# Performance work log

Hardware: AMD Instinct MI355X
Metric: run time of the kernel (lower is better)

The kernel has to match this reference:

```python
import jax, jax.numpy as jnp
import numpy as np

B, S, HID = 1, 4096, 2048
H, KV, D = 16, 8, 128
N_REP = H // KV
SCALING = float(128 ** -0.5)   # query_pre_attn_scalar ** -0.5
SOFTCAP = 50.0
WINDOW = 1024
NEG = -1e9


def setup_inputs() -> dict:
    key = jax.random.key(0)
    ks = jax.random.split(key, 6)
    hidden_states = jax.random.normal(ks[0], (B, S, HID), dtype=jnp.float32)
    Wq = jax.random.normal(ks[1], (HID, H * D), dtype=jnp.float32) * 0.02
    Wk = jax.random.normal(ks[2], (HID, KV * D), dtype=jnp.float32) * 0.02
    Wv = jax.random.normal(ks[3], (HID, KV * D), dtype=jnp.float32) * 0.02
    Wo = jax.random.normal(ks[4], (H * D, HID), dtype=jnp.float32) * 0.02
    # RoPE tables [1, S, D]
    inv_freq = 1.0 / (10000.0 ** (jnp.arange(0, D, 2, dtype=jnp.float32) / D))
    freqs = jnp.outer(jnp.arange(S, dtype=jnp.float32), inv_freq)   # [S, D/2]
    emb = jnp.concatenate([freqs, freqs], axis=-1)                  # [S, D]
    cos = jnp.cos(emb)[None]
    sin = jnp.sin(emb)[None]
    # causal + sliding-window additive mask [1, 1, S, S]
    i = jnp.arange(S)[:, None]
    j = jnp.arange(S)[None, :]
    allowed = (j <= i) & ((i - j) < WINDOW)
    attention_mask = jnp.where(allowed, 0.0, NEG).astype(jnp.float32)[None, None]
    return {"hidden_states": hidden_states, "cos": cos, "sin": sin,
            "attention_mask": attention_mask, "Wq": Wq, "Wk": Wk, "Wv": Wv, "Wo": Wo}


def _rotate_half(x):
    x1, x2 = jnp.split(x, 2, axis=-1)
    return jnp.concatenate([-x2, x1], axis=-1)


def reference(hidden_states, cos, sin, attention_mask, Wq, Wk, Wv, Wo):
    b, s, _ = hidden_states.shape
    # projections -> [B, heads, S, D]
    q = (hidden_states @ Wq).reshape(b, s, H, D).transpose(0, 2, 1, 3)
    k = (hidden_states @ Wk).reshape(b, s, KV, D).transpose(0, 2, 1, 3)
    v = (hidden_states @ Wv).reshape(b, s, KV, D).transpose(0, 2, 1, 3)
    # RoPE (unsqueeze_dim=1)
    c = cos[:, None]  # [B, 1, S, D]
    sn = sin[:, None]
    q = q * c + _rotate_half(q) * sn
    k = k * c + _rotate_half(k) * sn
    # repeat_kv (GQA)
    k = jnp.repeat(k, N_REP, axis=1)
    v = jnp.repeat(v, N_REP, axis=1)
    # scores with softcap + mask
    scores = jnp.einsum('bhqd,bhkd->bhqk', q, k) * SCALING
    scores = jnp.tanh(scores / SOFTCAP) * SOFTCAP
    scores = scores + attention_mask
    attn = jax.nn.softmax(scores.astype(jnp.float32), axis=-1).astype(q.dtype)
    out = jnp.einsum('bhqk,bhkd->bhqd', attn, v)
    out = out.transpose(0, 2, 1, 3).reshape(b, s, H * D)
    return out @ Wo
```

## Files before the change

### kernel.cpp

```cpp
#include <hip/hip_runtime.h>

#define S 4096
#define HID 2048
#define NH 16
#define NKV 8
#define HD 128
#define WINDOW 1024
#define SCALING 0.08838834764831845f
#define SOFTCAP 50.0f

typedef __bf16 bf16x8 __attribute__((ext_vector_type(8)));
typedef __bf16 bf16x4 __attribute__((ext_vector_type(4)));
typedef float f32x4 __attribute__((ext_vector_type(4)));

__device__ inline void gll16(const void* g, void* l) {
  __builtin_amdgcn_global_load_lds((const __attribute__((address_space(1))) void*)g,
                                   (__attribute__((address_space(3))) void*)l, 16, 0, 0);
}

__global__ void prep_all(const float* __restrict__ hs, __bf16* __restrict__ hsb,
                         const float* __restrict__ Wq, const float* __restrict__ Wk,
                         const float* __restrict__ Wv, const float* __restrict__ Wo,
                         __bf16* __restrict__ wqkvT, __bf16* __restrict__ woT) {
  int b = blockIdx.x;
  int t = threadIdx.x;
  if (b < 8192) {
    int i = b * 256 + t;
    float4 v = ((const float4*)hs)[i];
    bf16x4 o;
    o[0] = (__bf16)v.x; o[1] = (__bf16)v.y; o[2] = (__bf16)v.z; o[3] = (__bf16)v.w;
    ((bf16x4*)hsb)[i] = o;
    return;
  }
  __shared__ float tile[64][65];
  int y = b - 8192;
  int k0 = (y & 31) * 64;
  int wy = y >> 5;
  const float* src; __bf16* dst; int Nsrc, c0, perm, n0;
  if (wy < 32)      { src = Wq; dst = wqkvT; Nsrc = 2048; c0 = wy * 64;        perm = 1; n0 = wy * 64; }
  else if (wy < 48) { src = Wk; dst = wqkvT; Nsrc = 1024; c0 = (wy - 32) * 64; perm = 1; n0 = 2048 + (wy - 32) * 64; }
  else if (wy < 64) { src = Wv; dst = wqkvT; Nsrc = 1024; c0 = (wy - 48) * 64; perm = 0; n0 = 3072 + (wy - 48) * 64; }
  else              { src = Wo; dst = woT;   Nsrc = 2048; c0 = (wy - 64) * 64; perm = 0; n0 = (wy - 64) * 64; }
#pragma unroll
  for (int e = 0; e < 16; ++e) {
    int f = e * 256 + t; int r = f >> 6, c = f & 63;
    tile[r][c] = src[(size_t)(k0 + r) * Nsrc + c0 + c];
  }
  __syncthreads();
#pragma unroll
  for (int e = 0; e < 16; ++e) {
    int f = e * 256 + t; int r = f >> 6, c = f & 63;
    int n = n0 + r;
    if (perm) {
      int d = n & 127, o = d >> 4;
      int g = (o < 4) ? (o * 2) : ((o - 4) * 2 + 1);
      n = (n & ~127) | (g << 4) | (d & 15);
    }
    dst[(size_t)n * 2048 + k0 + c] = (__bf16)tile[c][r];
  }
}

__global__ __launch_bounds__(256) void gemm_qkv(const __bf16* __restrict__ A,
                                                const __bf16* __restrict__ B,
                                                __bf16* __restrict__ qr,
                                                __bf16* __restrict__ kr,
                                                __bf16* __restrict__ vt,
                                                const float* __restrict__ cosp,
                                                const float* __restrict__ sinp) {
  __shared__ __align__(16) __bf16 As[128 * 64];
  __shared__ __align__(16) __bf16 Bs[128 * 64];
  const int K = 2048;
  int m0 = blockIdx.x * 128, n0 = blockIdx.y * 128;
  int t = threadIdx.x;
  int lane = t & 63, wave = t >> 6;
  int wm = wave & 1, wn = wave >> 1;
  int quad = lane >> 4, l16 = lane & 15;

  f32x4 acc[4][4] = {};

  const __bf16* Abase = A + (size_t)m0 * K;
  const __bf16* Bbase = B + (size_t)n0 * K;

  for (int kk = 0; kk < K; kk += 64) {
    __syncthreads();
#pragma unroll
    for (int i = 0; i < 4; ++i) {
      int idx = i * 256 + t;
      int row = idx >> 3, c = idx & 7;
      int g = (c ^ (row & 7)) * 8;
      gll16(Abase + (size_t)row * K + kk + g, &As[idx * 8]);
      gll16(Bbase + (size_t)row * K + kk + g, &Bs[idx * 8]);
    }
    __syncthreads();
#pragma unroll
    for (int ks = 0; ks < 64; ks += 32) {
      bf16x8 af[4], bfr[4];
#pragma unroll
      for (int i = 0; i < 4; ++i) {
        int row = wm * 64 + i * 16 + l16;
        af[i] = *(const bf16x8*)&As[row * 64 + (((quad + (ks >> 3)) ^ (row & 7)) * 8)];
      }
#pragma unroll
      for (int j = 0; j < 4; ++j) {
        int row = wn * 64 + j * 16 + l16;
        bfr[j] = *(const bf16x8*)&Bs[row * 64 + (((quad + (ks >> 3)) ^ (row & 7)) * 8)];
      }
#pragma unroll
      for (int i = 0; i < 4; ++i)
#pragma unroll
        for (int j = 0; j < 4; ++j)
          acc[i][j] = __builtin_amdgcn_mfma_f32_16x16x32_bf16(af[i], bfr[j], acc[i][j], 0, 0, 0);
    }
  }

  if (n0 < 3072) {
    __bf16* dst = (n0 < 2048) ? (qr + (size_t)(n0 >> 7) * S * 128)
                              : (kr + (size_t)((n0 - 2048) >> 7) * S * 128);
#pragma unroll
    for (int i = 0; i < 4; ++i)
#pragma unroll
      for (int r = 0; r < 4; ++r) {
        int row = m0 + wm * 64 + i * 16 + quad * 4 + r;
#pragma unroll
        for (int jp = 0; jp < 2; ++jp) {
          int ifr = (wn * 2 + jp) * 16 + l16;
          float c = cosp[(size_t)row * 128 + ifr];
          float sn = sinp[(size_t)row * 128 + ifr];
          float lo = acc[i][2 * jp][r], hi = acc[i][2 * jp + 1][r];
          dst[(size_t)row * 128 + wn * 64 + jp * 32 + l16]      = (__bf16)(lo * c - hi * sn);
          dst[(size_t)row * 128 + wn * 64 + jp * 32 + 16 + l16] = (__bf16)(hi * c + lo * sn);
        }
      }
  } else {
    int vc0 = n0 - 3072;
#pragma unroll
    for (int i = 0; i < 4; ++i)
#pragma unroll
      for (int j = 0; j < 4; ++j) {
        int row_base = m0 + wm * 64 + i * 16 + quad * 4;
        int col = vc0 + wn * 64 + j * 16 + l16;
        bf16x4 ov;
#pragma unroll
        for (int r = 0; r < 4; ++r) ov[r] = (__bf16)acc[i][j][r];
        *(bf16x4*)&vt[(size_t)col * S + row_base] = ov;
      }
  }
}

template <typename OutT>
__global__ __launch_bounds__(256) void gemm_bt(const __bf16* __restrict__ A,
                                               const __bf16* __restrict__ B,
                                               OutT* __restrict__ C, int N, int K) {
  __shared__ __align__(16) __bf16 As[128 * 64];
  __shared__ __align__(16) __bf16 Bs[128 * 64];
  int m0 = blockIdx.x * 128, n0 = blockIdx.y * 128;
  int t = threadIdx.x;
  int lane = t & 63, wave = t >> 6;
  int wm = wave & 1, wn = wave >> 1;
  int quad = lane >> 4, l16 = lane & 15;

  f32x4 acc[4][4] = {};

  const __bf16* Abase = A + (size_t)m0 * K;
  const __bf16* Bbase = B + (size_t)n0 * K;

  for (int kk = 0; kk < K; kk += 64) {
    __syncthreads();
#pragma unroll
    for (int i = 0; i < 4; ++i) {
      int idx = i * 256 + t;
      int row = idx >> 3, c = idx & 7;
      int g = (c ^ (row & 7)) * 8;
      gll16(Abase + (size_t)row * K + kk + g, &As[idx * 8]);
      gll16(Bbase + (size_t)row * K + kk + g, &Bs[idx * 8]);
    }
    __syncthreads();
#pragma unroll
    for (int ks = 0; ks < 64; ks += 32) {
      bf16x8 af[4], bfr[4];
#pragma unroll
      for (int i = 0; i < 4; ++i) {
        int row = wm * 64 + i * 16 + l16;
        af[i] = *(const bf16x8*)&As[row * 64 + (((quad + (ks >> 3)) ^ (row & 7)) * 8)];
      }
#pragma unroll
      for (int j = 0; j < 4; ++j) {
        int row = wn * 64 + j * 16 + l16;
        bfr[j] = *(const bf16x8*)&Bs[row * 64 + (((quad + (ks >> 3)) ^ (row & 7)) * 8)];
      }
#pragma unroll
      for (int i = 0; i < 4; ++i)
#pragma unroll
        for (int j = 0; j < 4; ++j)
          acc[i][j] = __builtin_amdgcn_mfma_f32_16x16x32_bf16(af[i], bfr[j], acc[i][j], 0, 0, 0);
    }
  }
#pragma unroll
  for (int i = 0; i < 4; ++i)
#pragma unroll
    for (int j = 0; j < 4; ++j)
#pragma unroll
      for (int r = 0; r < 4; ++r) {
        int row = m0 + wm * 64 + i * 16 + quad * 4 + r;
        int col = n0 + wn * 64 + j * 16 + l16;
        C[(size_t)row * N + col] = (OutT)acc[i][j][r];
      }
}

__global__ __launch_bounds__(512) void attn(const __bf16* __restrict__ qr,
                                            const __bf16* __restrict__ kr,
                                            const __bf16* __restrict__ vt,
                                            __bf16* __restrict__ ao) {
  __shared__ __align__(16) __bf16 Ks[2][64 * 128];
  __shared__ __align__(16) __bf16 Vs[3][128 * 64];

  int kvh = blockIdx.x;
  int q0 = blockIdx.y * 128;
  int t = threadIdx.x, lane = t & 63, wave = t >> 6;
  int quad = lane >> 4, l16 = lane & 15;
  int h = kvh * 2 + (wave & 1);
  int qbase = q0 + (wave >> 1) * 32;

  bf16x8 qf[2][4];
#pragma unroll
  for (int mi = 0; mi < 2; ++mi) {
    const __bf16* qptr = qr + ((size_t)h * S + qbase + mi * 16 + l16) * 128;
#pragma unroll
    for (int ks = 0; ks < 4; ++ks)
      qf[mi][ks] = *(const bf16x8*)&qptr[ks * 32 + quad * 8];
  }

  f32x4 o[2][8] = {};
  float lpart[2] = {0.f, 0.f};

  int lo = q0 - (WINDOW - 1); if (lo < 0) lo = 0;
  int kt_begin = (lo / 64) * 64;
  int kt_end = q0 + 128;
  int NT = (kt_end - kt_begin) >> 6;

  const __bf16* kbase0 = kr + (size_t)kvh * S * 128;
  const __bf16* vbase0 = vt + (size_t)kvh * 128 * S;

  float4 k0r[2], k1r[2];
  float2 v0a[2], v0b[2], v1a[2], v1b[2];

  auto load_regs = [&](int kt, float4 (&krg)[2], float2 (&va)[2], float2 (&vb)[2]) {
    const __bf16* kb = kbase0 + (size_t)kt * 128;
    const __bf16* vptr = vbase0 + kt;
#pragma unroll
    for (int i = 0; i < 2; ++i) {
      int off = i * 512 + t;
      krg[i] = *(const float4*)(kb + (size_t)off * 8);
      int r = off >> 3, c = off & 7;
      int base0 = 32 * (c >> 2) + 4 * (c & 3);
      va[i] = *(const float2*)(vptr + (size_t)r * S + base0);
      vb[i] = *(const float2*)(vptr + (size_t)r * S + base0 + 16);
    }
  };
  auto write_lds = [&](int kslot, int vslot, float4 (&krg)[2], float2 (&va)[2], float2 (&vb)[2]) {
#pragma unroll
    for (int i = 0; i < 2; ++i) {
      int off = i * 512 + t;
      { int r = off >> 4, c = off & 15;
        *(float4*)&Ks[kslot][r * 128 + ((c ^ (r & 15)) * 8)] = krg[i]; }
      { int r = off >> 3, c = off & 7;
        float4 v = {va[i].x, va[i].y, vb[i].x, vb[i].y};
        *(float4*)&Vs[vslot][r * 64 + ((c ^ (r & 7)) * 8)] = v; }
    }
  };

  const float XS = SCALING / SOFTCAP;
  f32x4 sA[2][4], sB[2][4];

  auto activ = [&](int kt0) {
    return !(kt0 > qbase + 31 || kt0 + 63 < qbase - (WINDOW - 1));
  };

  auto step = [&](int tt, f32x4 (&SC)[2][4], f32x4 (&SP)[2][4], int vr, int vw,
                  float4 (&krl)[2], float2 (&val)[2], float2 (&vbl)[2],
                  float4 (&krs)[2], float2 (&vas)[2], float2 (&vbs)[2]) {
    if (tt < NT) {
      int kt0 = kt_begin + tt * 64;
      if (activ(kt0)) {
        int kslot = tt & 1;
#pragma unroll
        for (int mi = 0; mi < 2; ++mi)
#pragma unroll
          for (int nt = 0; nt < 4; ++nt) SC[mi][nt] = {};
        __builtin_amdgcn_s_setprio(1);
#pragma unroll
        for (int nt = 0; nt < 4; ++nt) {
#pragma unroll
          for (int ks = 0; ks < 4; ++ks) {
            bf16x8 kf = *(const bf16x8*)&Ks[kslot][(nt * 16 + l16) * 128 + (((ks * 4 + quad) ^ l16) * 8)];
            SC[0][nt] = __builtin_amdgcn_mfma_f32_16x16x32_bf16(kf, qf[0][ks], SC[0][nt], 0, 0, 0);
            SC[1][nt] = __builtin_amdgcn_mfma_f32_16x16x32_bf16(kf, qf[1][ks], SC[1][nt], 0, 0, 0);
          }
        }
        __builtin_amdgcn_s_setprio(0);
      }
    }

    if (tt + 2 < NT) load_regs(kt_begin + (tt + 2) * 64, krl, val, vbl);

    if (tt > 0) {
      int kt0c = kt_begin + (tt - 1) * 64;
      if (activ(kt0c)) {
        bf16x4 pk[2][4];
        bool interior = (kt0c + 63 <= qbase) && (kt0c >= qbase + 31 - (WINDOW - 1));
#pragma unroll
        for (int mi = 0; mi < 2; ++mi) {
          int irow = qbase + mi * 16 + l16;
#pragma unroll
          for (int nt = 0; nt < 4; ++nt)
#pragma unroll
            for (int r = 0; r < 4; ++r) {
              float x = SP[mi][nt][r] * XS;
              x = fminf(fmaxf(x, -0.25f), 0.25f);
              float x2 = x * x;
              float th = x * fmaf(x2, fmaf(x2, 0.13333333f, -0.33333333f), 1.0f);
              float pp = __builtin_amdgcn_exp2f(fmaf(th, 72.134752f, -72.134752f));
              if (!interior) {
                int j = kt0c + nt * 16 + quad * 4 + r;
                bool ok = (j <= irow) && (irow - j < WINDOW);
                pp = ok ? pp : 0.0f;
              }
              lpart[mi] += pp;
              pk[mi][nt][r] = (__bf16)pp;
            }
        }

        bf16x8 pB[2][2];
#pragma unroll
        for (int mi = 0; mi < 2; ++mi)
#pragma unroll
          for (int ks = 0; ks < 2; ++ks)
#pragma unroll
            for (int e = 0; e < 4; ++e) {
              pB[mi][ks][e]     = pk[mi][2 * ks][e];
              pB[mi][ks][4 + e] = pk[mi][2 * ks + 1][e];
            }

        __builtin_amdgcn_s_setprio(1);
#pragma unroll
        for (int dt = 0; dt < 8; ++dt) {
          int row = dt * 16 + l16;
#pragma unroll
          for (int ks = 0; ks < 2; ++ks) {
            bf16x8 vf = *(const bf16x8*)&Vs[vr][row * 64 + (((ks * 4 + quad) ^ (l16 & 7)) * 8)];
#pragma unroll
            for (int mi = 0; mi < 2; ++mi)
              o[mi][dt] = __builtin_amdgcn_mfma_f32_16x16x32_bf16(vf, pB[mi][ks], o[mi][dt], 0, 0, 0);
          }
        }
        __builtin_amdgcn_s_setprio(0);
      }
    }

    if (tt + 1 < NT) write_lds((tt + 1) & 1, vw, krs, vas, vbs);
    __syncthreads();
  };

  load_regs(kt_begin, k0r, v0a, v0b);
  write_lds(0, 0, k0r, v0a, v0b);
  if (NT > 1) load_regs(kt_begin + 64, k1r, v1a, v1b);
  __syncthreads();

  int vw = 1, vr = 2;
  for (int tt = 0; tt < NT; tt += 2) {
    step(tt, sA, sB, vr, vw, k0r, v0a, v0b, k1r, v1a, v1b);
    if (++vw == 3) vw = 0; if (++vr == 3) vr = 0;
    step(tt + 1, sB, sA, vr, vw, k1r, v1a, v1b, k0r, v0a, v0b);
    if (++vw == 3) vw = 0; if (++vr == 3) vr = 0;
  }
  step(NT, sA, sB, vr, vw, k0r, v0a, v0b, k1r, v1a, v1b);

#pragma unroll
  for (int mi = 0; mi < 2; ++mi) {
    float ls = lpart[mi];
    ls += __shfl_xor(ls, 16);
    ls += __shfl_xor(ls, 32);
    float inv = 1.f / ls;
    int row = qbase + mi * 16 + l16;
    __bf16* dst = ao + (size_t)row * (NH * HD) + h * HD + quad * 4;
#pragma unroll
    for (int dt = 0; dt < 8; ++dt) {
      bf16x4 ov;
#pragma unroll
      for (int r = 0; r < 4; ++r) ov[r] = (__bf16)(o[mi][dt][r] * inv);
      *(bf16x4*)(dst + dt * 16) = ov;
    }
  }
}

extern "C" void kernel_launch(void* const* d_in, const int* in_sizes, int n_in,
                              void* d_out, int out_size, void* d_ws, size_t ws_size,
                              hipStream_t stream) {
  const float* hs   = (const float*)d_in[0];
  const float* cosp = (const float*)d_in[1];
  const float* sinp = (const float*)d_in[2];
  const float* Wq = (const float*)d_in[4];
  const float* Wk = (const float*)d_in[5];
  const float* Wv = (const float*)d_in[6];
  const float* Wo = (const float*)d_in[7];
  float* out = (float*)d_out;

  char* w = (char*)d_ws;
  __bf16* hsb   = (__bf16*)w; w += (size_t)S * HID * 2;
  __bf16* wqkvT = (__bf16*)w; w += (size_t)4096 * 2048 * 2;
  __bf16* woT   = (__bf16*)w; w += (size_t)2048 * 2048 * 2;
  __bf16* qr    = (__bf16*)w; w += (size_t)NH * S * HD * 2;
  __bf16* kr    = (__bf16*)w; w += (size_t)NKV * S * HD * 2;
  __bf16* vtb   = (__bf16*)w; w += (size_t)NKV * HD * S * 2;
  __bf16* ao    = hsb;

  prep_all<<<8192 + 3072, 256, 0, stream>>>(hs, hsb, Wq, Wk, Wv, Wo, wqkvT, woT);

  gemm_qkv<<<dim3(32, 32), 256, 0, stream>>>(hsb, wqkvT, qr, kr, vtb, cosp, sinp);

  attn<<<dim3(NKV, 32), 512, 0, stream>>>(qr, kr, vtb, ao);

  gemm_bt<float><<<dim3(32, 16), 256, 0, stream>>>(ao, woT, out, 2048, 2048);
}
```

Before: 359.7 us.

## Enlarge QKV GEMM tile to 256x256 with double-buffered LDS pipeline

The QKV projection GEMM moves from 128x128 tiles with 4 waves to 256x256 tiles with 8 waves. LDS is double-buffered, and the loads for the next K tile are interleaved with MFMA phases, using s_setprio and barriers. The goal is to hide global-load latency and raise arithmetic intensity per block. In exchange, LDS use grows to 128KB and register pressure rises, and with only 256 blocks the launch may not fill all CUs evenly.

```diff
diff --git a/kernel.cpp b/kernel.cpp
--- a/kernel.cpp
+++ b/kernel.cpp
@@ -60,88 +60,129 @@
   }
 }
 
-__global__ __launch_bounds__(256) void gemm_qkv(const __bf16* __restrict__ A,
+__global__ __launch_bounds__(512) void gemm_qkv(const __bf16* __restrict__ A,
                                                 const __bf16* __restrict__ B,
                                                 __bf16* __restrict__ qr,
                                                 __bf16* __restrict__ kr,
                                                 __bf16* __restrict__ vt,
                                                 const float* __restrict__ cosp,
                                                 const float* __restrict__ sinp) {
-  __shared__ __align__(16) __bf16 As[128 * 64];
-  __shared__ __align__(16) __bf16 Bs[128 * 64];
+  __shared__ __align__(16) __bf16 As[2][2][128 * 64];
+  __shared__ __align__(16) __bf16 Bs[2][2][128 * 64];
   const int K = 2048;
-  int m0 = blockIdx.x * 128, n0 = blockIdx.y * 128;
+  const int NT = K / 64;
+  int m0 = blockIdx.x * 256, n0 = blockIdx.y * 256;
   int t = threadIdx.x;
   int lane = t & 63, wave = t >> 6;
   int wm = wave & 1, wn = wave >> 1;
   int quad = lane >> 4, l16 = lane & 15;
 
-  f32x4 acc[4][4] = {};
+  f32x4 acc[8][4] = {};
 
   const __bf16* Abase = A + (size_t)m0 * K;
   const __bf16* Bbase = B + (size_t)n0 * K;
 
-  for (int kk = 0; kk < K; kk += 64) {
-    __syncthreads();
-#pragma unroll
-    for (int i = 0; i < 4; ++i) {
-      int idx = i * 256 + t;
+  auto stageA = [&](int buf, int half, int kt) {
+    const __bf16* src = Abase + (size_t)(half * 128) * K + kt * 64;
+#pragma unroll
+    for (int j = 0; j < 2; ++j) {
+      int idx = j * 512 + t;
       int row = idx >> 3, c = idx & 7;
       int g = (c ^ (row & 7)) * 8;
-      gll16(Abase + (size_t)row * K + kk + g, &As[idx * 8]);
-      gll16(Bbase + (size_t)row * K + kk + g, &Bs[idx * 8]);
-    }
-    __syncthreads();
-#pragma unroll
-    for (int ks = 0; ks < 64; ks += 32) {
-      bf16x8 af[4], bfr[4];
-#pragma unroll
-      for (int i = 0; i < 4; ++i) {
-        int row = wm * 64 + i * 16 + l16;
-        af[i] = *(const bf16x8*)&As[row * 64 + (((quad + (ks >> 3)) ^ (row & 7)) * 8)];
-      }
-#pragma unroll
-      for (int j = 0; j < 4; ++j) {
-        int row = wn * 64 + j * 16 + l16;
-        bfr[j] = *(const bf16x8*)&Bs[row * 64 + (((quad + (ks >> 3)) ^ (row & 7)) * 8)];
-      }
-#pragma unroll
-      for (int i = 0; i < 4; ++i)
-#pragma unroll
-        for (int j = 0; j < 4; ++j)
-          acc[i][j] = __builtin_amdgcn_mfma_f32_16x16x32_bf16(af[i], bfr[j], acc[i][j], 0, 0, 0);
-    }
+      gll16(src + (size_t)row * K + g, &As[buf][half][idx * 8]);
+    }
+  };
+  auto stageB = [&](int buf, int half, int kt) {
+    const __bf16* src = Bbase + (size_t)(half * 128) * K + kt * 64;
+#pragma unroll
+    for (int j = 0; j < 2; ++j) {
+      int idx = j * 512 + t;
+      int row = idx >> 3, c = idx & 7;
+      int g = (c ^ (row & 7)) * 8;
+      gll16(src + (size_t)row * K + g, &Bs[buf][half][idx * 8]);
+    }
+  };
+
+  bf16x8 af[8];
+
+  auto readA = [&](int buf, int mi, int ks) -> bf16x8 {
+    int row = mi * 16 + l16;
+    return *(const bf16x8*)&As[buf][wm][row * 64 + (((quad + ks * 4) ^ (row & 7)) * 8)];
+  };
+  auto readB = [&](int buf, int ni, int ks) -> bf16x8 {
+    int row = (wn & 1) * 64 + ni * 16 + l16;
+    return *(const bf16x8*)&Bs[buf][wn >> 1][row * 64 + (((quad + ks * 4) ^ (row & 7)) * 8)];
+  };
+
+  auto phase = [&](int buf, int q, auto&& stage_fn) {
+    int ks = q >> 1, nip = q & 1;
+    if (nip == 0) {
+#pragma unroll
+      for (int mi = 0; mi < 8; ++mi) af[mi] = readA(buf, mi, ks);
+    }
+    bf16x8 b0 = readB(buf, 2 * nip, ks);
+    bf16x8 b1 = readB(buf, 2 * nip + 1, ks);
+    stage_fn();
+    __builtin_amdgcn_s_barrier();
+    __builtin_amdgcn_s_setprio(1);
+#pragma unroll
+    for (int mi = 0; mi < 8; ++mi) {
+      acc[mi][2 * nip]     = __builtin_amdgcn_mfma_f32_16x16x32_bf16(af[mi], b0, acc[mi][2 * nip], 0, 0, 0);
+      acc[mi][2 * nip + 1] = __builtin_amdgcn_mfma_f32_16x16x32_bf16(af[mi], b1, acc[mi][2 * nip + 1], 0, 0, 0);
+    }
+    __builtin_amdgcn_s_setprio(0);
+    __builtin_amdgcn_s_barrier();
+  };
+
+  stageA(0, 0, 0); stageA(0, 1, 0); stageB(0, 0, 0); stageB(0, 1, 0);
+  asm volatile("s_waitcnt vmcnt(0)" ::: "memory");
+  __builtin_amdgcn_s_barrier();
+  __builtin_amdgcn_sched_barrier(0);
+
+  for (int kt = 0; kt < NT; ++kt) {
+    int buf = kt & 1, nbuf = buf ^ 1;
+    bool st = (kt + 1 < NT);
+    int ktn = kt + 1;
+    phase(buf, 0, [&] { if (st) stageA(nbuf, 0, ktn); });
+    phase(buf, 1, [&] { if (st) stageA(nbuf, 1, ktn); });
+    phase(buf, 2, [&] { if (st) stageB(nbuf, 0, ktn); });
+    phase(buf, 3, [&] { if (st) stageB(nbuf, 1, ktn); });
+    asm volatile("s_waitcnt vmcnt(0)" ::: "memory");
+    __builtin_amdgcn_s_barrier();
+    __builtin_amdgcn_sched_barrier(0);
   }
 
   if (n0 < 3072) {
-    __bf16* dst = (n0 < 2048) ? (qr + (size_t)(n0 >> 7) * S * 128)
-                              : (kr + (size_t)((n0 - 2048) >> 7) * S * 128);
-#pragma unroll
-    for (int i = 0; i < 4; ++i)
+    int nf = n0 + wn * 64;
+    __bf16* dst = (n0 < 2048) ? (qr + (size_t)(nf >> 7) * S * 128)
+                              : (kr + (size_t)((nf - 2048) >> 7) * S * 128);
+    int colb = nf & 64;
+#pragma unroll
+    for (int mi = 0; mi < 8; ++mi)
 #pragma unroll
       for (int r = 0; r < 4; ++r) {
-        int row = m0 + wm * 64 + i * 16 + quad * 4 + r;
+        int row = m0 + wm * 128 + mi * 16 + quad * 4 + r;
 #pragma unroll
         for (int jp = 0; jp < 2; ++jp) {
-          int ifr = (wn * 2 + jp) * 16 + l16;
+          int ifr = ((wn & 1) * 2 + jp) * 16 + l16;
           float c = cosp[(size_t)row * 128 + ifr];
           float sn = sinp[(size_t)row * 128 + ifr];
-          float lo = acc[i][2 * jp][r], hi = acc[i][2 * jp + 1][r];
-          dst[(size_t)row * 128 + wn * 64 + jp * 32 + l16]      = (__bf16)(lo * c - hi * sn);
-          dst[(size_t)row * 128 + wn * 64 + jp * 32 + 16 + l16] = (__bf16)(hi * c + lo * sn);
+          float lo = acc[mi][2 * jp][r], hi = acc[mi][2 * jp + 1][r];
+          dst[(size_t)row * 128 + colb + jp * 32 + l16]      = (__bf16)(lo * c - hi * sn);
+          dst[(size_t)row * 128 + colb + jp * 32 + 16 + l16] = (__bf16)(hi * c + lo * sn);
         }
       }
   } else {
     int vc0 = n0 - 3072;
 #pragma unroll
-    for (int i = 0; i < 4; ++i)
-#pragma unroll
-      for (int j = 0; j < 4; ++j) {
-        int row_base = m0 + wm * 64 + i * 16 + quad * 4;
-        int col = vc0 + wn * 64 + j * 16 + l16;
+    for (int mi = 0; mi < 8; ++mi)
+#pragma unroll
+      for (int ni = 0; ni < 4; ++ni) {
+        int row_base = m0 + wm * 128 + mi * 16 + quad * 4;
+        int col = vc0 + wn * 64 + ni * 16 + l16;
         bf16x4 ov;
 #pragma unroll
-        for (int r = 0; r < 4; ++r) ov[r] = (__bf16)acc[i][j][r];
+        for (int r = 0; r < 4; ++r) ov[r] = (__bf16)acc[mi][ni][r];
         *(bf16x4*)&vt[(size_t)col * S + row_base] = ov;
       }
   }
@@ -416,7 +457,7 @@
 
   prep_all<<<8192 + 3072, 256, 0, stream>>>(hs, hsb, Wq, Wk, Wv, Wo, wqkvT, woT);
 
-  gemm_qkv<<<dim3(32, 32), 256, 0, stream>>>(hsb, wqkvT, qr, kr, vtb, cosp, sinp);
+  gemm_qkv<<<dim3(16, 16), 512, 0, stream>>>(hsb, wqkvT, qr, kr, vtb, cosp, sinp);
 
   attn<<<dim3(NKV, 32), 512, 0, stream>>>(qr, kr, vtb, ao);
 
```

Result: no change. 356.4 us (-0.9%).
